# Kernel optimization log

Hardware: AMD Instinct MI355X
Metric: run time of the kernel (lower is better)

The kernel has to match this reference:

```python
import jax, jax.numpy as jnp
import numpy as np

B = 8192; N = 50; NUM_NODES = 200000; NUM_EDGES = 1000000
FEAT = 64; EFEAT = 4; TD = 16; D = 64


def setup_inputs() -> dict:
    key = jax.random.key(0)
    ks = jax.random.split(key, 32)
    p = lambda i, shape: jax.random.normal(ks[i], shape, jnp.float32) * 0.05
    inp = {}
    nf = jax.random.normal(ks[0], (NUM_NODES, FEAT), jnp.float32)
    skills = jax.random.randint(ks[1], (NUM_NODES,), 0, 100).astype(jnp.float32)
    inp['node_raw_features'] = nf.at[:, 0].set(skills)  # col 0 = skill id
    inp['edge_raw_features'] = jax.random.normal(ks[2], (NUM_EDGES, EFEAT), jnp.float32)
    inp['src_node_ids'] = jax.random.randint(ks[3], (B,), 0, NUM_NODES)
    inp['dst_node_ids'] = jax.random.randint(ks[4], (B,), 0, NUM_NODES)
    inp['node_interact_times'] = jax.random.uniform(ks[5], (B,), jnp.float32, 0.0, 1e4)
    inp['src_neighbor_node_ids'] = jax.random.randint(ks[6], (B, N), 0, NUM_NODES)
    inp['src_neighbor_edge_ids'] = jax.random.randint(ks[7], (B, N), 0, NUM_EDGES)
    inp['src_neighbor_times'] = jax.random.uniform(ks[8], (B, N), jnp.float32, 0.0, 1e4)
    inp['dst_neighbor_node_ids'] = jax.random.randint(ks[9], (B, N), 0, NUM_NODES)
    inp['dst_neighbor_edge_ids'] = jax.random.randint(ks[10], (B, N), 0, NUM_EDGES)
    inp['dst_neighbor_times'] = jax.random.uniform(ks[11], (B, N), jnp.float32, 0.0, 1e4)
    # projection layers
    inp['W_feat'] = p(12, (FEAT, D)); inp['b_feat'] = p(13, (D,))
    inp['W_edge'] = p(14, (1, D));    inp['b_edge'] = p(15, (D,))
    inp['W_time'] = p(16, (TD, D));   inp['b_time'] = p(17, (D,))
    inp['W_struct'] = p(18, (1, D));  inp['b_struct'] = p(19, (D,))
    inp['W_out'] = p(20, (D, D));     inp['b_out'] = p(21, (D,))
    # time encoder (cos(w*dt + b), trainable Linear(1, TD) as in TGN TimeEncoder)
    inp['time_w'] = p(22, (TD,)); inp['time_b'] = p(23, (TD,))
    # src / dst GRUs (PyTorch layout: W_ih [3H,E], W_hh [3H,H])
    inp['src_W_ih'] = p(24, (3 * D, D)); inp['src_W_hh'] = p(25, (3 * D, D))
    inp['src_b_ih'] = p(26, (3 * D,));   inp['src_b_hh'] = p(27, (3 * D,))
    inp['dst_W_ih'] = p(28, (3 * D, D)); inp['dst_W_hh'] = p(29, (3 * D, D))
    inp['dst_b_ih'] = p(30, (3 * D,));   inp['dst_b_hh'] = p(31, (3 * D,))
    return inp


def _lin(x, W, b):
    return x @ W + b


def _gru_last_hidden(x, W_ih, W_hh, b_ih, b_hh):
    # x: [B, T, E] -> final hidden state [B, H] (PyTorch GRU equations)
    Bb, _, _ = x.shape
    H = W_hh.shape[1]

    def step(h, xt):
        gi = xt @ W_ih.T + b_ih            # [B, 3H]
        gh = h @ W_hh.T + b_hh             # [B, 3H]
        ir, iz, inn = jnp.split(gi, 3, axis=-1)
        hr, hz, hn = jnp.split(gh, 3, axis=-1)
        r = jax.nn.sigmoid(ir + hr)
        z = jax.nn.sigmoid(iz + hz)
        n = jnp.tanh(inn + r * hn)
        h_new = (1.0 - z) * n + z * h
        return h_new, None

    h0 = jnp.zeros((Bb, H), x.dtype)
    hT, _ = jax.lax.scan(step, h0, jnp.swapaxes(x, 0, 1))
    return hT


def reference(node_raw_features, edge_raw_features, src_node_ids, dst_node_ids,
              node_interact_times, src_neighbor_node_ids, src_neighbor_edge_ids,
              src_neighbor_times, dst_neighbor_node_ids, dst_neighbor_edge_ids,
              dst_neighbor_times, W_feat, b_feat, W_edge, b_edge, W_time, b_time,
              W_struct, b_struct, W_out, b_out, time_w, time_b,
              src_W_ih, src_W_hh, src_b_ih, src_b_hh,
              dst_W_ih, dst_W_hh, dst_b_ih, dst_b_hh):
    t = node_interact_times
    # append the query interaction itself (edge id 0) -> [B, N+1]
    src_nids = jnp.concatenate([src_neighbor_node_ids, src_node_ids[:, None]], 1)
    src_eids = jnp.concatenate([src_neighbor_edge_ids, jnp.zeros_like(src_node_ids)[:, None]], 1)
    src_ts = jnp.concatenate([src_neighbor_times, t[:, None]], 1)
    dst_nids = jnp.concatenate([dst_neighbor_node_ids, dst_node_ids[:, None]], 1)
    dst_eids = jnp.concatenate([dst_neighbor_edge_ids, jnp.zeros_like(dst_node_ids)[:, None]], 1)
    dst_ts = jnp.concatenate([dst_neighbor_times, t[:, None]], 1)

    # co-occurrence features [B, N, 1]
    co_src = (src_neighbor_node_ids == dst_node_ids[:, None]).astype(jnp.float32)[..., None]
    co_dst = (dst_neighbor_node_ids == src_node_ids[:, None]).astype(jnp.float32)[..., None]
    # skill match features [B, N, 1]
    src_skill = node_raw_features[src_nids][:, :-1, 0].astype(jnp.int32)
    dst_skill = node_raw_features[dst_nids][:, -1, 0].astype(jnp.int32)[:, None]
    skill_f = (src_skill == dst_skill).astype(jnp.float32)[..., None]

    src_struct = _lin(co_src, W_struct, b_struct)
    dst_struct = _lin(co_dst, W_struct, b_struct)
    skill_struct = _lin(skill_f, W_struct, b_struct)

    def get_feats(nids, eids, ts):
        node_f = _lin(node_raw_features[nids], W_feat, b_feat)        # [B,N+1,D]
        delta = t[:, None] - ts                                       # dual-decay ablation: delta times
        tenc = jnp.cos(delta[..., None] * time_w + time_b)            # [B,N+1,TD]
        time_f = _lin(tenc, W_time, b_time)                           # [B,N+1,D]
        edge_f = _lin(edge_raw_features[eids][..., :1], W_edge, b_edge)
        return node_f, edge_f, time_f

    sn, se, st = get_feats(src_nids, src_eids, src_ts)
    dn, de, dt = get_feats(dst_nids, dst_eids, dst_ts)
    src_feats = sn + se + st
    dst_feats = dn + de + dt

    src_emb = _gru_last_hidden(src_feats[:, :-1] + skill_struct + src_struct,
                               src_W_ih, src_W_hh, src_b_ih, src_b_hh) + (se + st)[:, -1]
    dst_emb = _gru_last_hidden((de + dt)[:, :-1] + dst_struct,
                               dst_W_ih, dst_W_hh, dst_b_ih, dst_b_hh) + dst_feats[:, -1]

    return _lin(src_emb, W_out, b_out), _lin(dst_emb, W_out, b_out)
```

## Files before the change

### kernel.cpp

```cpp
#include <hip/hip_runtime.h>
#include <stdint.h>

#define BB 8192
#define NN 50

typedef _Float16 half8 __attribute__((ext_vector_type(8)));
typedef float floatx4 __attribute__((ext_vector_type(4)));

union FragU { uint4 u; half8 h; };
static __device__ __forceinline__ half8 u2h(uint4 u) { FragU f; f.u = u; return f.h; }

static __device__ __forceinline__ uint32_t pk2u(float a, float b) {
    auto p = __builtin_amdgcn_cvt_pkrtz(a, b);
    uint32_t u; __builtin_memcpy(&u, &p, 4); return u;
}

#define MFMA(A, B, C) __builtin_amdgcn_mfma_f32_16x16x32_f16((A), (B), (C), 0, 0, 0)

static __device__ __forceinline__ float fsig(float x)   { return 1.0f / (1.0f + __expf(-x)); }
static __device__ __forceinline__ float ftanhf(float x) { return 1.0f - 2.0f / (__expf(2.0f * x) + 1.0f); }

__global__ __launch_bounds__(256, 1)
void dygkt3(const float* __restrict__ nodef, const float* __restrict__ edgef,
            const int* __restrict__ src_ids, const int* __restrict__ dst_ids,
            const float* __restrict__ times,
            const int* __restrict__ s_nids, const int* __restrict__ s_eids,
            const float* __restrict__ s_ts,
            const int* __restrict__ d_nids, const int* __restrict__ d_eids,
            const float* __restrict__ d_ts,
            const float* __restrict__ W_feat, const float* __restrict__ b_feat,
            const float* __restrict__ W_edge, const float* __restrict__ b_edge,
            const float* __restrict__ W_time, const float* __restrict__ b_time,
            const float* __restrict__ W_str,  const float* __restrict__ b_str,
            const float* __restrict__ W_out,  const float* __restrict__ b_out,
            const float* __restrict__ time_w, const float* __restrict__ time_b,
            const float* __restrict__ sWih, const float* __restrict__ sWhh,
            const float* __restrict__ sbih, const float* __restrict__ sbhh,
            const float* __restrict__ dWih, const float* __restrict__ dWhh,
            const float* __restrict__ dbih, const float* __restrict__ dbhh,
            float* __restrict__ out)
{
    __shared__ uint4 wfA[8][64];
    __shared__ uint4 woA[8][64];
    __shared__ __align__(16) _Float16 xbuf[4][16 * 72];
    __shared__ __align__(16) _Float16 hbuf[4][16 * 72];

    const int tid = threadIdx.x, wave = tid >> 6, lane = tid & 63;
    const int g = lane >> 4, i16 = lane & 15;
    const bool is_src = blockIdx.x < 128;
    const int ib0 = (int)(blockIdx.x & 127) * 64 + wave * 16;
    const int b = ib0 + i16;

    for (int q = tid; q < 512; q += 256) {
        int l = q & 63, tt = q >> 6;
        int kh = tt >> 2, mt = tt & 3, gg = l >> 4, ii = l & 15;
        float v[8], w[8];
        #pragma unroll
        for (int j = 0; j < 8; ++j) {
            int k = 32 * kh + 8 * gg + j, m = 16 * mt + ii;
            v[j] = W_feat[k * 64 + m];
            w[j] = W_out[k * 64 + m];
        }
        wfA[tt][l] = make_uint4(pk2u(v[0],v[1]), pk2u(v[2],v[3]), pk2u(v[4],v[5]), pk2u(v[6],v[7]));
        woA[tt][l] = make_uint4(pk2u(w[0],w[1]), pk2u(w[2],w[3]), pk2u(w[4],w[5]), pk2u(w[6],w[7]));
    }
    for (int q = tid; q < 4 * 16 * 72 / 2; q += 256) ((uint32_t*)hbuf)[q] = 0;
    __syncthreads();

    const float* WI = is_src ? sWih : dWih;
    const float* WH = is_src ? sWhh : dWhh;
    uint4 wih[12][2], whh[12][2];
    #pragma unroll
    for (int mt = 0; mt < 12; ++mt)
        #pragma unroll
        for (int kh = 0; kh < 2; ++kh) {
            const float* p = WI + (size_t)(16 * mt + i16) * 64 + 32 * kh + 8 * g;
            float4 a = *(const float4*)p, c = *(const float4*)(p + 4);
            wih[mt][kh] = make_uint4(pk2u(a.x,a.y), pk2u(a.z,a.w), pk2u(c.x,c.y), pk2u(c.z,c.w));
            const float* q = WH + (size_t)(16 * mt + i16) * 64 + 32 * kh + 8 * g;
            float4 e = *(const float4*)q, f = *(const float4*)(q + 4);
            whh[mt][kh] = make_uint4(pk2u(e.x,e.y), pk2u(e.z,e.w), pk2u(f.x,f.y), pk2u(f.z,f.w));
        }

    uint4 wtA[4];
    #pragma unroll
    for (int mt = 0; mt < 4; ++mt) {
        float v[8];
        #pragma unroll
        for (int j = 0; j < 8; ++j) {
            int k = 8 * g + j, dim = 16 * mt + i16;
            float x = 0.0f;
            if (k < 16)       x = W_time[k * 64 + dim];
            else if (k == 16) x = W_edge[dim];
            else if (k == 17) x = W_str[dim];
            else if (k == 18) x = b_edge[dim] + b_time[dim];
            else if (k == 19) x = is_src ? (b_feat[dim] + 2.0f * b_str[dim]) : b_str[dim];
            else if (k == 20) x = b_feat[dim];
            v[j] = x;
        }
        wtA[mt] = make_uint4(pk2u(v[0],v[1]), pk2u(v[2],v[3]), pk2u(v[4],v[5]), pk2u(v[6],v[7]));
    }

    const float* BI = is_src ? sbih : dbih;
    const float* BH = is_src ? sbhh : dbhh;
    floatx4 brz[8], bin[4], bhn[4];
    #pragma unroll
    for (int mt = 0; mt < 8; ++mt) {
        floatx4 v;
        #pragma unroll
        for (int r = 0; r < 4; ++r) v[r] = BI[16 * mt + 4 * g + r] + BH[16 * mt + 4 * g + r];
        brz[mt] = v;
    }
    #pragma unroll
    for (int mt = 0; mt < 4; ++mt) {
        floatx4 vi, vh;
        #pragma unroll
        for (int r = 0; r < 4; ++r) {
            vi[r] = BI[128 + 16 * mt + 4 * g + r];
            vh[r] = BH[128 + 16 * mt + 4 * g + r];
        }
        bin[mt] = vi; bhn[mt] = vh;
    }

    const int* pn = (is_src ? s_nids : d_nids) + (size_t)b * NN;
    const int* pe = (is_src ? s_eids : d_eids) + (size_t)b * NN;
    const float* pt = (is_src ? s_ts : d_ts) + (size_t)b * NN;
    const float tqL = times[b];
    const int didL = dst_ids[b];
    const int oid = is_src ? didL : src_ids[b];
    const float dskill = is_src ? nodef[(size_t)didL * 64] : 0.0f;
    float twc[8], tbc[8];
    #pragma unroll
    for (int j = 0; j < 8; ++j) {
        int k = 8 * (g & 1) + j;
        twc[j] = time_w[k]; tbc[j] = time_b[k];
    }

    int nidC = pn[0], eidC = pe[0];
    float tsC = pt[0];
    float e0C = edgef[4 * (size_t)eidC];
    float4 nfa = {0,0,0,0}, nfb = {0,0,0,0}, nfc = {0,0,0,0}, nfd = {0,0,0,0};
    if (is_src) {
        const float* rp = nodef + (size_t)nidC * 64 + 8 * g;
        nfa = *(const float4*)rp;        nfb = *(const float4*)(rp + 4);
        nfc = *(const float4*)(rp + 32); nfd = *(const float4*)(rp + 36);
    }

    floatx4 hM[4] = {{0,0,0,0},{0,0,0,0},{0,0,0,0},{0,0,0,0}};
    const floatx4 z4 = {0,0,0,0};
    _Float16* xb = xbuf[wave];
    _Float16* hb = hbuf[wave];

    for (int t = 0; t < NN; ++t) {
        int nidN = 0, eidN = 0; float tsN = 0.0f;
        if (t + 1 < NN) { nidN = pn[t + 1]; eidN = pe[t + 1]; tsN = pt[t + 1]; }

        float nsk = __shfl(nfa.x, i16);
        float sf = ((nidC == oid) ? 1.0f : 0.0f) +
                   ((is_src && nsk == dskill) ? 1.0f : 0.0f);
        float delta = tqL - tsC;
        uint4 tb4;
        if (g < 2) {
            float cv[8];
            #pragma unroll
            for (int j = 0; j < 8; ++j) cv[j] = __cosf(delta * twc[j] + tbc[j]);
            tb4 = make_uint4(pk2u(cv[0],cv[1]), pk2u(cv[2],cv[3]), pk2u(cv[4],cv[5]), pk2u(cv[6],cv[7]));
        } else if (g == 2) {
            tb4 = make_uint4(pk2u(e0C, sf), pk2u(1.0f, 1.0f), 0u, 0u);
        } else {
            tb4 = make_uint4(0u, 0u, 0u, 0u);
        }
        half8 tB = u2h(tb4);

        floatx4 xacc[4];
        if (is_src) {
            uint4 nf0 = make_uint4(pk2u(nfa.x,nfa.y), pk2u(nfa.z,nfa.w), pk2u(nfb.x,nfb.y), pk2u(nfb.z,nfb.w));
            uint4 nf1 = make_uint4(pk2u(nfc.x,nfc.y), pk2u(nfc.z,nfc.w), pk2u(nfd.x,nfd.y), pk2u(nfd.z,nfd.w));
            half8 nB0 = u2h(nf0), nB1 = u2h(nf1);
            #pragma unroll
            for (int mt = 0; mt < 4; ++mt) {
                floatx4 a = MFMA(u2h(wfA[mt][lane]), nB0, z4);
                a = MFMA(u2h(wfA[4 + mt][lane]), nB1, a);
                xacc[mt] = MFMA(u2h(wtA[mt]), tB, a);
            }
        } else {
            #pragma unroll
            for (int mt = 0; mt < 4; ++mt) xacc[mt] = MFMA(u2h(wtA[mt]), tB, z4);
        }

        #pragma unroll
        for (int mt = 0; mt < 4; ++mt)
            *(uint2*)&xb[i16 * 72 + mt * 16 + 4 * g] =
                make_uint2(pk2u(xacc[mt][0], xacc[mt][1]), pk2u(xacc[mt][2], xacc[mt][3]));
        half8 xB0 = u2h(*(const uint4*)&xb[i16 * 72 + 8 * g]);
        half8 xB1 = u2h(*(const uint4*)&xb[i16 * 72 + 32 + 8 * g]);

        float e0N = 0.0f; float4 na = {0,0,0,0}, nb = {0,0,0,0}, nc = {0,0,0,0}, nd = {0,0,0,0};
        if (t + 1 < NN) {
            e0N = edgef[4 * (size_t)eidN];
            if (is_src) {
                const float* rp = nodef + (size_t)nidN * 64 + 8 * g;
                na = *(const float4*)rp;        nb = *(const float4*)(rp + 4);
                nc = *(const float4*)(rp + 32); nd = *(const float4*)(rp + 36);
            }
        }

        half8 hB0 = u2h(*(const uint4*)&hb[i16 * 72 + 8 * g]);
        half8 hB1 = u2h(*(const uint4*)&hb[i16 * 72 + 32 + 8 * g]);

        floatx4 rg[4], zg[4], ia[4], ha[4];
        #pragma unroll
        for (int mt = 0; mt < 4; ++mt) {
            floatx4 a = MFMA(u2h(wih[mt][0]), xB0, brz[mt]);
            a = MFMA(u2h(wih[mt][1]), xB1, a);
            a = MFMA(u2h(whh[mt][0]), hB0, a);
            rg[mt] = MFMA(u2h(whh[mt][1]), hB1, a);
        }
        #pragma unroll
        for (int mt = 0; mt < 4; ++mt) {
            floatx4 a = MFMA(u2h(wih[4 + mt][0]), xB0, brz[4 + mt]);
            a = MFMA(u2h(wih[4 + mt][1]), xB1, a);
            a = MFMA(u2h(whh[4 + mt][0]), hB0, a);
            zg[mt] = MFMA(u2h(whh[4 + mt][1]), hB1, a);
        }
        #pragma unroll
        for (int mt = 0; mt < 4; ++mt) {
            floatx4 a = MFMA(u2h(wih[8 + mt][0]), xB0, bin[mt]);
            ia[mt] = MFMA(u2h(wih[8 + mt][1]), xB1, a);
            floatx4 c = MFMA(u2h(whh[8 + mt][0]), hB0, bhn[mt]);
            ha[mt] = MFMA(u2h(whh[8 + mt][1]), hB1, c);
        }

        #pragma unroll
        for (int mt = 0; mt < 4; ++mt)
            #pragma unroll
            for (int r = 0; r < 4; ++r) {
                float rr = fsig(rg[mt][r]);
                float zz = fsig(zg[mt][r]);
                float nn = ftanhf(ia[mt][r] + rr * ha[mt][r]);
                hM[mt][r] = nn + zz * (hM[mt][r] - nn);
            }

        #pragma unroll
        for (int mt = 0; mt < 4; ++mt)
            *(uint2*)&hb[i16 * 72 + mt * 16 + 4 * g] =
                make_uint2(pk2u(hM[mt][0], hM[mt][1]), pk2u(hM[mt][2], hM[mt][3]));

        nidC = nidN; eidC = eidN; tsC = tsN; e0C = e0N;
        nfa = na; nfb = nb; nfc = nc; nfd = nd;
    }

    float e00 = edgef[0];
    uint4 tt4;
    if (g < 2) {
        float cv[8];
        #pragma unroll
        for (int j = 0; j < 8; ++j) cv[j] = __cosf(tbc[j]);
        tt4 = make_uint4(pk2u(cv[0],cv[1]), pk2u(cv[2],cv[3]), pk2u(cv[4],cv[5]), pk2u(cv[6],cv[7]));
    } else if (g == 2) {
        tt4 = make_uint4(pk2u(e00, 0.0f), pk2u(1.0f, 0.0f), pk2u(is_src ? 0.0f : 1.0f, 0.0f), 0u);
    } else {
        tt4 = make_uint4(0u, 0u, 0u, 0u);
    }
    half8 tT = u2h(tt4);

    floatx4 tacc[4];
    #pragma unroll
    for (int mt = 0; mt < 4; ++mt) tacc[mt] = MFMA(u2h(wtA[mt]), tT, z4);
    if (!is_src) {
        const float* rp = nodef + (size_t)didL * 64 + 8 * g;
        float4 da = *(const float4*)rp,        db = *(const float4*)(rp + 4);
        float4 dc = *(const float4*)(rp + 32), dd = *(const float4*)(rp + 36);
        uint4 d0 = make_uint4(pk2u(da.x,da.y), pk2u(da.z,da.w), pk2u(db.x,db.y), pk2u(db.z,db.w));
        uint4 d1 = make_uint4(pk2u(dc.x,dc.y), pk2u(dc.z,dc.w), pk2u(dd.x,dd.y), pk2u(dd.z,dd.w));
        #pragma unroll
        for (int mt = 0; mt < 4; ++mt) {
            tacc[mt] = MFMA(u2h(wfA[mt][lane]), u2h(d0), tacc[mt]);
            tacc[mt] = MFMA(u2h(wfA[4 + mt][lane]), u2h(d1), tacc[mt]);
        }
    }

    #pragma unroll
    for (int mt = 0; mt < 4; ++mt) {
        floatx4 e = hM[mt] + tacc[mt];
        *(uint2*)&xb[i16 * 72 + mt * 16 + 4 * g] =
            make_uint2(pk2u(e[0], e[1]), pk2u(e[2], e[3]));
    }
    half8 eB0 = u2h(*(const uint4*)&xb[i16 * 72 + 8 * g]);
    half8 eB1 = u2h(*(const uint4*)&xb[i16 * 72 + 32 + 8 * g]);

    const size_t obase = (is_src ? 0 : (size_t)BB * 64) + (size_t)(ib0 + i16) * 64;
    #pragma unroll
    for (int mt = 0; mt < 4; ++mt) {
        floatx4 bo;
        #pragma unroll
        for (int r = 0; r < 4; ++r) bo[r] = b_out[16 * mt + 4 * g + r];
        floatx4 o = MFMA(u2h(woA[mt][lane]), eB0, bo);
        o = MFMA(u2h(woA[4 + mt][lane]), eB1, o);
        #pragma unroll
        for (int r = 0; r < 4; ++r)
            out[obase + 16 * mt + 4 * g + r] = o[r];
    }
}

extern "C" void kernel_launch(void* const* d_in, const int* in_sizes, int n_in,
                              void* d_out, int out_size, void* d_ws, size_t ws_size,
                              hipStream_t stream) {
    (void)in_sizes; (void)n_in; (void)d_ws; (void)ws_size; (void)out_size;
    const float* nodef  = (const float*)d_in[0];
    const float* edgef  = (const float*)d_in[1];
    const int*   srcid  = (const int*)  d_in[2];
    const int*   dstid  = (const int*)  d_in[3];
    const float* times  = (const float*)d_in[4];
    const int*   s_nids = (const int*)  d_in[5];
    const int*   s_eids = (const int*)  d_in[6];
    const float* s_ts   = (const float*)d_in[7];
    const int*   d_nids = (const int*)  d_in[8];
    const int*   d_eids = (const int*)  d_in[9];
    const float* d_ts   = (const float*)d_in[10];
    const float* W_feat = (const float*)d_in[11];
    const float* b_feat = (const float*)d_in[12];
    const float* W_edge = (const float*)d_in[13];
    const float* b_edge = (const float*)d_in[14];
    const float* W_time = (const float*)d_in[15];
    const float* b_time = (const float*)d_in[16];
    const float* W_str  = (const float*)d_in[17];
    const float* b_str  = (const float*)d_in[18];
    const float* W_out  = (const float*)d_in[19];
    const float* b_out  = (const float*)d_in[20];
    const float* time_w = (const float*)d_in[21];
    const float* time_b = (const float*)d_in[22];
    const float* sWih   = (const float*)d_in[23];
    const float* sWhh   = (const float*)d_in[24];
    const float* sbih   = (const float*)d_in[25];
    const float* sbhh   = (const float*)d_in[26];
    const float* dWih   = (const float*)d_in[27];
    const float* dWhh   = (const float*)d_in[28];
    const float* dbih   = (const float*)d_in[29];
    const float* dbhh   = (const float*)d_in[30];

    dim3 grid(256), block(256);
    dygkt3<<<grid, block, 0, stream>>>(
        nodef, edgef, srcid, dstid, times,
        s_nids, s_eids, s_ts, d_nids, d_eids, d_ts,
        W_feat, b_feat, W_edge, b_edge, W_time, b_time,
        W_str, b_str, W_out, b_out, time_w, time_b,
        sWih, sWhh, sbih, sbhh, dWih, dWhh, dbih, dbhh,
        (float*)d_out);
}
```

Baseline: 300.4 us.

## Split each 16-row GRU batch across two waves with ping-pong LDS hidden state

Each 16-sample batch tile is now handled by a pair of waves. Each wave computes half of the 64 hidden units for every gate, and the halves are exchanged through double-buffered LDS with one barrier per timestep. This halves the per-wave MFMA chain on the serial recurrence and the register-resident weights, so more waves can run in parallel (1024 blocks of 128 threads, 2 blocks per CU). The cost is a block barrier every step. The change also switches sigmoid/tanh to exp2/rcp intrinsics and vectorizes the output store.

Measured after the change: 245.5 us. -18.3%, faster.

```diff
diff --git a/kernel.cpp b/kernel.cpp
--- a/kernel.cpp
+++ b/kernel.cpp
@@ -17,11 +17,30 @@
 
 #define MFMA(A, B, C) __builtin_amdgcn_mfma_f32_16x16x32_f16((A), (B), (C), 0, 0, 0)
 
-static __device__ __forceinline__ float fsig(float x)   { return 1.0f / (1.0f + __expf(-x)); }
-static __device__ __forceinline__ float ftanhf(float x) { return 1.0f - 2.0f / (__expf(2.0f * x) + 1.0f); }
-
-__global__ __launch_bounds__(256, 1)
-void dygkt3(const float* __restrict__ nodef, const float* __restrict__ edgef,
+static __device__ __forceinline__ float frcp(float x) {
+#if __has_builtin(__builtin_amdgcn_rcpf)
+    return __builtin_amdgcn_rcpf(x);
+#else
+    return 1.0f / x;
+#endif
+}
+static __device__ __forceinline__ float fexp2(float x) {
+#if __has_builtin(__builtin_amdgcn_exp2f)
+    return __builtin_amdgcn_exp2f(x);
+#else
+    return __expf(0.69314718056f * x);
+#endif
+}
+static __device__ __forceinline__ float fsig(float x)   { return frcp(1.0f + fexp2(-1.44269504089f * x)); }
+static __device__ __forceinline__ float ftanhf(float x) { return 1.0f - 2.0f * frcp(fexp2(2.88539008178f * x) + 1.0f); }
+
+static __device__ __forceinline__ void bar_lds() {
+    asm volatile("s_waitcnt lgkmcnt(0)" ::: "memory");
+    __builtin_amdgcn_s_barrier();
+}
+
+__global__ __launch_bounds__(128, 2)
+void dygkt4(const float* __restrict__ nodef, const float* __restrict__ edgef,
             const int* __restrict__ src_ids, const int* __restrict__ dst_ids,
             const float* __restrict__ times,
             const int* __restrict__ s_nids, const int* __restrict__ s_eids,
@@ -42,49 +61,53 @@
 {
     __shared__ uint4 wfA[8][64];
     __shared__ uint4 woA[8][64];
-    __shared__ __align__(16) _Float16 xbuf[4][16 * 72];
-    __shared__ __align__(16) _Float16 hbuf[4][16 * 72];
-
-    const int tid = threadIdx.x, wave = tid >> 6, lane = tid & 63;
+    __shared__ __align__(16) _Float16 xls[2][16 * 72];
+    __shared__ __align__(16) _Float16 hls[2][16 * 72];
+
+    const int tid = threadIdx.x, w = tid >> 6, lane = tid & 63;
     const int g = lane >> 4, i16 = lane & 15;
-    const bool is_src = blockIdx.x < 128;
-    const int ib0 = (int)(blockIdx.x & 127) * 64 + wave * 16;
+    const bool is_src = blockIdx.x < 512;
+    const int ib0 = (int)(blockIdx.x & 511) * 16;
     const int b = ib0 + i16;
 
-    for (int q = tid; q < 512; q += 256) {
+    for (int q = tid; q < 512; q += 128) {
         int l = q & 63, tt = q >> 6;
         int kh = tt >> 2, mt = tt & 3, gg = l >> 4, ii = l & 15;
-        float v[8], w[8];
+        float v[8], u[8];
         #pragma unroll
         for (int j = 0; j < 8; ++j) {
             int k = 32 * kh + 8 * gg + j, m = 16 * mt + ii;
             v[j] = W_feat[k * 64 + m];
-            w[j] = W_out[k * 64 + m];
+            u[j] = W_out[k * 64 + m];
         }
         wfA[tt][l] = make_uint4(pk2u(v[0],v[1]), pk2u(v[2],v[3]), pk2u(v[4],v[5]), pk2u(v[6],v[7]));
-        woA[tt][l] = make_uint4(pk2u(w[0],w[1]), pk2u(w[2],w[3]), pk2u(w[4],w[5]), pk2u(w[6],w[7]));
-    }
-    for (int q = tid; q < 4 * 16 * 72 / 2; q += 256) ((uint32_t*)hbuf)[q] = 0;
+        woA[tt][l] = make_uint4(pk2u(u[0],u[1]), pk2u(u[2],u[3]), pk2u(u[4],u[5]), pk2u(u[6],u[7]));
+    }
+    for (int q = tid; q < 16 * 72 / 2; q += 128) ((uint32_t*)hls[0])[q] = 0u;
     __syncthreads();
 
     const float* WI = is_src ? sWih : dWih;
     const float* WH = is_src ? sWhh : dWhh;
-    uint4 wih[12][2], whh[12][2];
-    #pragma unroll
-    for (int mt = 0; mt < 12; ++mt)
-        #pragma unroll
-        for (int kh = 0; kh < 2; ++kh) {
-            const float* p = WI + (size_t)(16 * mt + i16) * 64 + 32 * kh + 8 * g;
-            float4 a = *(const float4*)p, c = *(const float4*)(p + 4);
-            wih[mt][kh] = make_uint4(pk2u(a.x,a.y), pk2u(a.z,a.w), pk2u(c.x,c.y), pk2u(c.z,c.w));
-            const float* q = WH + (size_t)(16 * mt + i16) * 64 + 32 * kh + 8 * g;
-            float4 e = *(const float4*)q, f = *(const float4*)(q + 4);
-            whh[mt][kh] = make_uint4(pk2u(e.x,e.y), pk2u(e.z,e.w), pk2u(f.x,f.y), pk2u(f.z,f.w));
-        }
-
-    uint4 wtA[4];
-    #pragma unroll
-    for (int mt = 0; mt < 4; ++mt) {
+    uint4 wih[6][2], whh[6][2];
+    #pragma unroll
+    for (int gt = 0; gt < 3; ++gt)
+        #pragma unroll
+        for (int tq = 0; tq < 2; ++tq)
+            #pragma unroll
+            for (int kh = 0; kh < 2; ++kh) {
+                int row = 64 * gt + 16 * (2 * w + tq) + i16;
+                const float* p = WI + (size_t)row * 64 + 32 * kh + 8 * g;
+                float4 a = *(const float4*)p, c = *(const float4*)(p + 4);
+                wih[gt * 2 + tq][kh] = make_uint4(pk2u(a.x,a.y), pk2u(a.z,a.w), pk2u(c.x,c.y), pk2u(c.z,c.w));
+                const float* qq = WH + (size_t)row * 64 + 32 * kh + 8 * g;
+                float4 e = *(const float4*)qq, f = *(const float4*)(qq + 4);
+                whh[gt * 2 + tq][kh] = make_uint4(pk2u(e.x,e.y), pk2u(e.z,e.w), pk2u(f.x,f.y), pk2u(f.z,f.w));
+            }
+
+    uint4 wtA[2];
+    #pragma unroll
+    for (int tq = 0; tq < 2; ++tq) {
+        int mt = 2 * w + tq;
         float v[8];
         #pragma unroll
         for (int j = 0; j < 8; ++j) {
@@ -98,28 +121,29 @@
             else if (k == 20) x = b_feat[dim];
             v[j] = x;
         }
-        wtA[mt] = make_uint4(pk2u(v[0],v[1]), pk2u(v[2],v[3]), pk2u(v[4],v[5]), pk2u(v[6],v[7]));
+        wtA[tq] = make_uint4(pk2u(v[0],v[1]), pk2u(v[2],v[3]), pk2u(v[4],v[5]), pk2u(v[6],v[7]));
     }
 
     const float* BI = is_src ? sbih : dbih;
     const float* BH = is_src ? sbhh : dbhh;
-    floatx4 brz[8], bin[4], bhn[4];
-    #pragma unroll
-    for (int mt = 0; mt < 8; ++mt) {
-        floatx4 v;
-        #pragma unroll
-        for (int r = 0; r < 4; ++r) v[r] = BI[16 * mt + 4 * g + r] + BH[16 * mt + 4 * g + r];
-        brz[mt] = v;
-    }
-    #pragma unroll
-    for (int mt = 0; mt < 4; ++mt) {
+    floatx4 brz[4], bin[2], bhn[2];
+    #pragma unroll
+    for (int gz = 0; gz < 2; ++gz)
+        #pragma unroll
+        for (int tq = 0; tq < 2; ++tq) {
+            int r0 = 64 * gz + 16 * (2 * w + tq) + 4 * g;
+            floatx4 v;
+            #pragma unroll
+            for (int r = 0; r < 4; ++r) v[r] = BI[r0 + r] + BH[r0 + r];
+            brz[gz * 2 + tq] = v;
+        }
+    #pragma unroll
+    for (int tq = 0; tq < 2; ++tq) {
+        int r0 = 128 + 16 * (2 * w + tq) + 4 * g;
         floatx4 vi, vh;
         #pragma unroll
-        for (int r = 0; r < 4; ++r) {
-            vi[r] = BI[128 + 16 * mt + 4 * g + r];
-            vh[r] = BH[128 + 16 * mt + 4 * g + r];
-        }
-        bin[mt] = vi; bhn[mt] = vh;
+        for (int r = 0; r < 4; ++r) { vi[r] = BI[r0 + r]; vh[r] = BH[r0 + r]; }
+        bin[tq] = vi; bhn[tq] = vh;
     }
 
     const int* pn = (is_src ? s_nids : d_nids) + (size_t)b * NN;
@@ -146,10 +170,9 @@
         nfc = *(const float4*)(rp + 32); nfd = *(const float4*)(rp + 36);
     }
 
-    floatx4 hM[4] = {{0,0,0,0},{0,0,0,0},{0,0,0,0},{0,0,0,0}};
+    floatx4 hM[2] = {{0,0,0,0},{0,0,0,0}};
     const floatx4 z4 = {0,0,0,0};
-    _Float16* xb = xbuf[wave];
-    _Float16* hb = hbuf[wave];
+    int cur = 0;
 
     for (int t = 0; t < NN; ++t) {
         int nidN = 0, eidN = 0; float tsN = 0.0f;
@@ -172,28 +195,27 @@
         }
         half8 tB = u2h(tb4);
 
-        floatx4 xacc[4];
+        floatx4 xacc[2];
         if (is_src) {
             uint4 nf0 = make_uint4(pk2u(nfa.x,nfa.y), pk2u(nfa.z,nfa.w), pk2u(nfb.x,nfb.y), pk2u(nfb.z,nfb.w));
             uint4 nf1 = make_uint4(pk2u(nfc.x,nfc.y), pk2u(nfc.z,nfc.w), pk2u(nfd.x,nfd.y), pk2u(nfd.z,nfd.w));
             half8 nB0 = u2h(nf0), nB1 = u2h(nf1);
             #pragma unroll
-            for (int mt = 0; mt < 4; ++mt) {
+            for (int tq = 0; tq < 2; ++tq) {
+                int mt = 2 * w + tq;
                 floatx4 a = MFMA(u2h(wfA[mt][lane]), nB0, z4);
                 a = MFMA(u2h(wfA[4 + mt][lane]), nB1, a);
-                xacc[mt] = MFMA(u2h(wtA[mt]), tB, a);
+                xacc[tq] = MFMA(u2h(wtA[tq]), tB, a);
             }
         } else {
             #pragma unroll
-            for (int mt = 0; mt < 4; ++mt) xacc[mt] = MFMA(u2h(wtA[mt]), tB, z4);
-        }
-
-        #pragma unroll
-        for (int mt = 0; mt < 4; ++mt)
-            *(uint2*)&xb[i16 * 72 + mt * 16 + 4 * g] =
-                make_uint2(pk2u(xacc[mt][0], xacc[mt][1]), pk2u(xacc[mt][2], xacc[mt][3]));
-        half8 xB0 = u2h(*(const uint4*)&xb[i16 * 72 + 8 * g]);
-        half8 xB1 = u2h(*(const uint4*)&xb[i16 * 72 + 32 + 8 * g]);
+            for (int tq = 0; tq < 2; ++tq) xacc[tq] = MFMA(u2h(wtA[tq]), tB, z4);
+        }
+
+        #pragma unroll
+        for (int tq = 0; tq < 2; ++tq)
+            *(uint2*)&xls[cur][i16 * 72 + 32 * w + 16 * tq + 4 * g] =
+                make_uint2(pk2u(xacc[tq][0], xacc[tq][1]), pk2u(xacc[tq][2], xacc[tq][3]));
 
         float e0N = 0.0f; float4 na = {0,0,0,0}, nb = {0,0,0,0}, nc = {0,0,0,0}, nd = {0,0,0,0};
         if (t + 1 < NN) {
@@ -205,47 +227,52 @@
             }
         }
 
-        half8 hB0 = u2h(*(const uint4*)&hb[i16 * 72 + 8 * g]);
-        half8 hB1 = u2h(*(const uint4*)&hb[i16 * 72 + 32 + 8 * g]);
-
-        floatx4 rg[4], zg[4], ia[4], ha[4];
-        #pragma unroll
-        for (int mt = 0; mt < 4; ++mt) {
-            floatx4 a = MFMA(u2h(wih[mt][0]), xB0, brz[mt]);
-            a = MFMA(u2h(wih[mt][1]), xB1, a);
-            a = MFMA(u2h(whh[mt][0]), hB0, a);
-            rg[mt] = MFMA(u2h(whh[mt][1]), hB1, a);
-        }
-        #pragma unroll
-        for (int mt = 0; mt < 4; ++mt) {
-            floatx4 a = MFMA(u2h(wih[4 + mt][0]), xB0, brz[4 + mt]);
-            a = MFMA(u2h(wih[4 + mt][1]), xB1, a);
-            a = MFMA(u2h(whh[4 + mt][0]), hB0, a);
-            zg[mt] = MFMA(u2h(whh[4 + mt][1]), hB1, a);
-        }
-        #pragma unroll
-        for (int mt = 0; mt < 4; ++mt) {
-            floatx4 a = MFMA(u2h(wih[8 + mt][0]), xB0, bin[mt]);
-            ia[mt] = MFMA(u2h(wih[8 + mt][1]), xB1, a);
-            floatx4 c = MFMA(u2h(whh[8 + mt][0]), hB0, bhn[mt]);
-            ha[mt] = MFMA(u2h(whh[8 + mt][1]), hB1, c);
-        }
-
-        #pragma unroll
-        for (int mt = 0; mt < 4; ++mt)
+        bar_lds();
+
+        half8 xB0 = u2h(*(const uint4*)&xls[cur][i16 * 72 + 8 * g]);
+        half8 xB1 = u2h(*(const uint4*)&xls[cur][i16 * 72 + 32 + 8 * g]);
+        half8 hB0 = u2h(*(const uint4*)&hls[cur][i16 * 72 + 8 * g]);
+        half8 hB1 = u2h(*(const uint4*)&hls[cur][i16 * 72 + 32 + 8 * g]);
+
+        floatx4 rg[2], zg[2], ia[2], ha[2];
+        #pragma unroll
+        for (int tq = 0; tq < 2; ++tq) {
+            floatx4 a = MFMA(u2h(wih[tq][0]), xB0, brz[tq]);
+            a = MFMA(u2h(wih[tq][1]), xB1, a);
+            a = MFMA(u2h(whh[tq][0]), hB0, a);
+            rg[tq] = MFMA(u2h(whh[tq][1]), hB1, a);
+        }
+        #pragma unroll
+        for (int tq = 0; tq < 2; ++tq) {
+            floatx4 a = MFMA(u2h(wih[2 + tq][0]), xB0, brz[2 + tq]);
+            a = MFMA(u2h(wih[2 + tq][1]), xB1, a);
+            a = MFMA(u2h(whh[2 + tq][0]), hB0, a);
+            zg[tq] = MFMA(u2h(whh[2 + tq][1]), hB1, a);
+        }
+        #pragma unroll
+        for (int tq = 0; tq < 2; ++tq) {
+            floatx4 a = MFMA(u2h(wih[4 + tq][0]), xB0, bin[tq]);
+            ia[tq] = MFMA(u2h(wih[4 + tq][1]), xB1, a);
+            floatx4 c = MFMA(u2h(whh[4 + tq][0]), hB0, bhn[tq]);
+            ha[tq] = MFMA(u2h(whh[4 + tq][1]), hB1, c);
+        }
+
+        #pragma unroll
+        for (int tq = 0; tq < 2; ++tq)
             #pragma unroll
             for (int r = 0; r < 4; ++r) {
-                float rr = fsig(rg[mt][r]);
-                float zz = fsig(zg[mt][r]);
-                float nn = ftanhf(ia[mt][r] + rr * ha[mt][r]);
-                hM[mt][r] = nn + zz * (hM[mt][r] - nn);
+                float rr = fsig(rg[tq][r]);
+                float zz = fsig(zg[tq][r]);
+                float nn = ftanhf(ia[tq][r] + rr * ha[tq][r]);
+                hM[tq][r] = nn + zz * (hM[tq][r] - nn);
             }
 
         #pragma unroll
-        for (int mt = 0; mt < 4; ++mt)
-            *(uint2*)&hb[i16 * 72 + mt * 16 + 4 * g] =
-                make_uint2(pk2u(hM[mt][0], hM[mt][1]), pk2u(hM[mt][2], hM[mt][3]));
-
+        for (int tq = 0; tq < 2; ++tq)
+            *(uint2*)&hls[cur ^ 1][i16 * 72 + 32 * w + 16 * tq + 4 * g] =
+                make_uint2(pk2u(hM[tq][0], hM[tq][1]), pk2u(hM[tq][2], hM[tq][3]));
+
+        cur ^= 1;
         nidC = nidN; eidC = eidN; tsC = tsN; e0C = e0N;
         nfa = na; nfb = nb; nfc = nc; nfd = nd;
     }
@@ -264,9 +291,9 @@
     }
     half8 tT = u2h(tt4);
 
-    floatx4 tacc[4];
-    #pragma unroll
-    for (int mt = 0; mt < 4; ++mt) tacc[mt] = MFMA(u2h(wtA[mt]), tT, z4);
+    floatx4 tacc[2];
+    #pragma unroll
+    for (int tq = 0; tq < 2; ++tq) tacc[tq] = MFMA(u2h(wtA[tq]), tT, z4);
     if (!is_src) {
         const float* rp = nodef + (size_t)didL * 64 + 8 * g;
         float4 da = *(const float4*)rp,        db = *(const float4*)(rp + 4);
@@ -274,32 +301,33 @@
         uint4 d0 = make_uint4(pk2u(da.x,da.y), pk2u(da.z,da.w), pk2u(db.x,db.y), pk2u(db.z,db.w));
         uint4 d1 = make_uint4(pk2u(dc.x,dc.y), pk2u(dc.z,dc.w), pk2u(dd.x,dd.y), pk2u(dd.z,dd.w));
         #pragma unroll
-        for (int mt = 0; mt < 4; ++mt) {
-            tacc[mt] = MFMA(u2h(wfA[mt][lane]), u2h(d0), tacc[mt]);
-            tacc[mt] = MFMA(u2h(wfA[4 + mt][lane]), u2h(d1), tacc[mt]);
-        }
-    }
-
-    #pragma unroll
-    for (int mt = 0; mt < 4; ++mt) {
-        floatx4 e = hM[mt] + tacc[mt];
-        *(uint2*)&xb[i16 * 72 + mt * 16 + 4 * g] =
+        for (int tq = 0; tq < 2; ++tq) {
+            int mt = 2 * w + tq;
+            tacc[tq] = MFMA(u2h(wfA[mt][lane]), u2h(d0), tacc[tq]);
+            tacc[tq] = MFMA(u2h(wfA[4 + mt][lane]), u2h(d1), tacc[tq]);
+        }
+    }
+
+    #pragma unroll
+    for (int tq = 0; tq < 2; ++tq) {
+        floatx4 e = hM[tq] + tacc[tq];
+        *(uint2*)&xls[0][i16 * 72 + 32 * w + 16 * tq + 4 * g] =
             make_uint2(pk2u(e[0], e[1]), pk2u(e[2], e[3]));
     }
-    half8 eB0 = u2h(*(const uint4*)&xb[i16 * 72 + 8 * g]);
-    half8 eB1 = u2h(*(const uint4*)&xb[i16 * 72 + 32 + 8 * g]);
-
-    const size_t obase = (is_src ? 0 : (size_t)BB * 64) + (size_t)(ib0 + i16) * 64;
-    #pragma unroll
-    for (int mt = 0; mt < 4; ++mt) {
+    bar_lds();
+    half8 eB0 = u2h(*(const uint4*)&xls[0][i16 * 72 + 8 * g]);
+    half8 eB1 = u2h(*(const uint4*)&xls[0][i16 * 72 + 32 + 8 * g]);
+
+    const size_t obase = (is_src ? 0 : (size_t)BB * 64) + (size_t)b * 64;
+    #pragma unroll
+    for (int tq = 0; tq < 2; ++tq) {
+        int mt = 2 * w + tq;
         floatx4 bo;
         #pragma unroll
         for (int r = 0; r < 4; ++r) bo[r] = b_out[16 * mt + 4 * g + r];
         floatx4 o = MFMA(u2h(woA[mt][lane]), eB0, bo);
         o = MFMA(u2h(woA[4 + mt][lane]), eB1, o);
-        #pragma unroll
-        for (int r = 0; r < 4; ++r)
-            out[obase + 16 * mt + 4 * g + r] = o[r];
+        *(floatx4*)(out + obase + 16 * mt + 4 * g) = o;
     }
 }
 
@@ -339,8 +367,8 @@
     const float* dbih   = (const float*)d_in[29];
     const float* dbhh   = (const float*)d_in[30];
 
-    dim3 grid(256), block(256);
-    dygkt3<<<grid, block, 0, stream>>>(
+    dim3 grid(1024), block(128);
+    dygkt4<<<grid, block, 0, stream>>>(
         nodef, edgef, srcid, dstid, times,
         s_nids, s_eids, s_ts, d_nids, d_eids, d_ts,
         W_feat, b_feat, W_edge, b_edge, W_time, b_time,
```

## Halve per-wave batch to 8 rows, move W_ih to LDS, fold gate scales into weights

Applied to the files above, without the earlier changes.

Each wave now handles 8 batch rows instead of 16, so the grid doubles to 512 blocks and launch bounds allow 2 blocks per CU. This trades wasted MFMA columns for more parallelism on the sequential GRU recurrence. W_ih, the time/edge weights and the biases move from registers to shared memory to free VGPRs. The sigmoid and tanh scale factors (log2e) are folded into the weights and biases so gates use raw exp2 and rcp builtins. Other changes: the output projection reads W_out from global memory directly, and the dst node row is prefetched in the last loop iteration.

After: 737.6 us. 146% more time.

```diff
diff --git a/kernel.cpp b/kernel.cpp
--- a/kernel.cpp
+++ b/kernel.cpp
@@ -17,11 +17,23 @@
 
 #define MFMA(A, B, C) __builtin_amdgcn_mfma_f32_16x16x32_f16((A), (B), (C), 0, 0, 0)
 
-static __device__ __forceinline__ float fsig(float x)   { return 1.0f / (1.0f + __expf(-x)); }
-static __device__ __forceinline__ float ftanhf(float x) { return 1.0f - 2.0f / (__expf(2.0f * x) + 1.0f); }
-
-__global__ __launch_bounds__(256, 1)
-void dygkt3(const float* __restrict__ nodef, const float* __restrict__ edgef,
+static __device__ __forceinline__ float frcp(float x) {
+#if __has_builtin(__builtin_amdgcn_rcpf)
+    return __builtin_amdgcn_rcpf(x);
+#else
+    return 1.0f / x;
+#endif
+}
+static __device__ __forceinline__ float fexp2(float x) {
+#if __has_builtin(__builtin_amdgcn_exp2f)
+    return __builtin_amdgcn_exp2f(x);
+#else
+    return __expf(0.69314718056f * x);
+#endif
+}
+
+__global__ __launch_bounds__(256, 2)
+void dygkt9(const float* __restrict__ nodef, const float* __restrict__ edgef,
             const int* __restrict__ src_ids, const int* __restrict__ dst_ids,
             const float* __restrict__ times,
             const int* __restrict__ s_nids, const int* __restrict__ s_eids,
@@ -40,55 +52,44 @@
             const float* __restrict__ dbih, const float* __restrict__ dbhh,
             float* __restrict__ out)
 {
+    __shared__ uint4 wihL[24][64];
     __shared__ uint4 wfA[8][64];
-    __shared__ uint4 woA[8][64];
-    __shared__ __align__(16) _Float16 xbuf[4][16 * 72];
-    __shared__ __align__(16) _Float16 hbuf[4][16 * 72];
-
-    const int tid = threadIdx.x, wave = tid >> 6, lane = tid & 63;
-    const int g = lane >> 4, i16 = lane & 15;
-    const bool is_src = blockIdx.x < 128;
-    const int ib0 = (int)(blockIdx.x & 127) * 64 + wave * 16;
-    const int b = ib0 + i16;
+    __shared__ uint4 wtAL[4][64];
+    __shared__ floatx4 biasL[16][4];
+    __shared__ __align__(16) _Float16 xtr[4][9 * 72];
+    __shared__ __align__(16) _Float16 htr[4][9 * 72];
+
+    const int tid = threadIdx.x, w = tid >> 6, lane = tid & 63;
+    const int g = lane >> 4, i16 = lane & 15, i8 = lane & 7;
+    const int ri = (i16 < 8) ? i16 : 8;
+    const bool is_src = (blockIdx.x & 1) == 0;
+    const int b = (int)(blockIdx.x >> 1) * 32 + w * 8 + i8;
+
+    const float SRZ = -1.44269504089f;
+    const float SN  =  2.88539008178f;
+    const floatx4 z4 = {0, 0, 0, 0};
+
+    const float* WI = is_src ? sWih : dWih;
+    const float* WH = is_src ? sWhh : dWhh;
+    const float* BI = is_src ? sbih : dbih;
+    const float* BH = is_src ? sbhh : dbhh;
 
     for (int q = tid; q < 512; q += 256) {
         int l = q & 63, tt = q >> 6;
         int kh = tt >> 2, mt = tt & 3, gg = l >> 4, ii = l & 15;
-        float v[8], w[8];
+        float v[8];
+        #pragma unroll
+        for (int j = 0; j < 8; ++j)
+            v[j] = W_feat[(32 * kh + 8 * gg + j) * 64 + 16 * mt + ii];
+        wfA[tt][l] = make_uint4(pk2u(v[0],v[1]), pk2u(v[2],v[3]), pk2u(v[4],v[5]), pk2u(v[6],v[7]));
+    }
+    {
+        int l = tid & 63, mt = tid >> 6;
+        int gg = l >> 4, ii = l & 15;
+        float v[8];
         #pragma unroll
         for (int j = 0; j < 8; ++j) {
-            int k = 32 * kh + 8 * gg + j, m = 16 * mt + ii;
-            v[j] = W_feat[k * 64 + m];
-            w[j] = W_out[k * 64 + m];
-        }
-        wfA[tt][l] = make_uint4(pk2u(v[0],v[1]), pk2u(v[2],v[3]), pk2u(v[4],v[5]), pk2u(v[6],v[7]));
-        woA[tt][l] = make_uint4(pk2u(w[0],w[1]), pk2u(w[2],w[3]), pk2u(w[4],w[5]), pk2u(w[6],w[7]));
-    }
-    for (int q = tid; q < 4 * 16 * 72 / 2; q += 256) ((uint32_t*)hbuf)[q] = 0;
-    __syncthreads();
-
-    const float* WI = is_src ? sWih : dWih;
-    const float* WH = is_src ? sWhh : dWhh;
-    uint4 wih[12][2], whh[12][2];
-    #pragma unroll
-    for (int mt = 0; mt < 12; ++mt)
-        #pragma unroll
-        for (int kh = 0; kh < 2; ++kh) {
-            const float* p = WI + (size_t)(16 * mt + i16) * 64 + 32 * kh + 8 * g;
-            float4 a = *(const float4*)p, c = *(const float4*)(p + 4);
-            wih[mt][kh] = make_uint4(pk2u(a.x,a.y), pk2u(a.z,a.w), pk2u(c.x,c.y), pk2u(c.z,c.w));
-            const float* q = WH + (size_t)(16 * mt + i16) * 64 + 32 * kh + 8 * g;
-            float4 e = *(const float4*)q, f = *(const float4*)(q + 4);
-            whh[mt][kh] = make_uint4(pk2u(e.x,e.y), pk2u(e.z,e.w), pk2u(f.x,f.y), pk2u(f.z,f.w));
-        }
-
-    uint4 wtA[4];
-    #pragma unroll
-    for (int mt = 0; mt < 4; ++mt) {
-        float v[8];
-        #pragma unroll
-        for (int j = 0; j < 8; ++j) {
-            int k = 8 * g + j, dim = 16 * mt + i16;
+            int k = 8 * gg + j, dim = 16 * mt + ii;
             float x = 0.0f;
             if (k < 16)       x = W_time[k * 64 + dim];
             else if (k == 16) x = W_edge[dim];
@@ -98,28 +99,51 @@
             else if (k == 20) x = b_feat[dim];
             v[j] = x;
         }
-        wtA[mt] = make_uint4(pk2u(v[0],v[1]), pk2u(v[2],v[3]), pk2u(v[4],v[5]), pk2u(v[6],v[7]));
-    }
-
-    const float* BI = is_src ? sbih : dbih;
-    const float* BH = is_src ? sbhh : dbhh;
-    floatx4 brz[8], bin[4], bhn[4];
-    #pragma unroll
-    for (int mt = 0; mt < 8; ++mt) {
+        wtAL[mt][l] = make_uint4(pk2u(v[0],v[1]), pk2u(v[2],v[3]), pk2u(v[4],v[5]), pk2u(v[6],v[7]));
+    }
+    for (int q = tid; q < 1536; q += 256) {
+        int l = q & 63, idx = q >> 6;
+        int gt = idx >> 3, rem = idx & 7, mt = rem >> 1, kh = rem & 1;
+        float s = (gt == 2) ? SN : SRZ;
+        int gg = l >> 4, ii = l & 15;
+        int row = 64 * gt + 16 * mt + ii;
+        const float* p = WI + (size_t)row * 64 + 32 * kh + 8 * gg;
+        float4 a = *(const float4*)p, c = *(const float4*)(p + 4);
+        wihL[idx][l] = make_uint4(pk2u(s*a.x,s*a.y), pk2u(s*a.z,s*a.w),
+                                  pk2u(s*c.x,s*c.y), pk2u(s*c.z,s*c.w));
+    }
+    if (tid < 64) {
+        int idx = tid >> 2, gg = tid & 3;
+        int which = idx >> 2, mt = idx & 3;
+        int base = 16 * mt + 4 * gg;
         floatx4 v;
         #pragma unroll
-        for (int r = 0; r < 4; ++r) v[r] = BI[16 * mt + 4 * g + r] + BH[16 * mt + 4 * g + r];
-        brz[mt] = v;
-    }
-    #pragma unroll
-    for (int mt = 0; mt < 4; ++mt) {
-        floatx4 vi, vh;
-        #pragma unroll
         for (int r = 0; r < 4; ++r) {
-            vi[r] = BI[128 + 16 * mt + 4 * g + r];
-            vh[r] = BH[128 + 16 * mt + 4 * g + r];
-        }
-        bin[mt] = vi; bhn[mt] = vh;
+            float x;
+            if (which == 0)      x = SRZ * (BI[base + r] + BH[base + r]);
+            else if (which == 1) x = SRZ * (BI[64 + base + r] + BH[64 + base + r]);
+            else if (which == 2) x = SN * BI[128 + base + r];
+            else                 x = SN * BH[128 + base + r];
+            v[r] = x;
+        }
+        biasL[idx][gg] = v;
+    }
+    for (int q = tid; q < 4 * 9 * 72 / 2; q += 256) ((uint32_t*)htr)[q] = 0u;
+
+    uint4 whh[3][4][2];
+    #pragma unroll
+    for (int gt = 0; gt < 3; ++gt) {
+        const float s = (gt == 2) ? SN : SRZ;
+        #pragma unroll
+        for (int mt = 0; mt < 4; ++mt)
+            #pragma unroll
+            for (int kh = 0; kh < 2; ++kh) {
+                int row = 64 * gt + 16 * mt + i16;
+                const float* p = WH + (size_t)row * 64 + 32 * kh + 8 * g;
+                float4 a = *(const float4*)p, c = *(const float4*)(p + 4);
+                whh[gt][mt][kh] = make_uint4(pk2u(s*a.x,s*a.y), pk2u(s*a.z,s*a.w),
+                                             pk2u(s*c.x,s*c.y), pk2u(s*c.z,s*c.w));
+            }
     }
 
     const int* pn = (is_src ? s_nids : d_nids) + (size_t)b * NN;
@@ -136,6 +160,8 @@
         twc[j] = time_w[k]; tbc[j] = time_b[k];
     }
 
+    __syncthreads();
+
     int nidC = pn[0], eidC = pe[0];
     float tsC = pt[0];
     float e0C = edgef[4 * (size_t)eidC];
@@ -146,16 +172,15 @@
         nfc = *(const float4*)(rp + 32); nfd = *(const float4*)(rp + 36);
     }
 
-    floatx4 hM[4] = {{0,0,0,0},{0,0,0,0},{0,0,0,0},{0,0,0,0}};
-    const floatx4 z4 = {0,0,0,0};
-    _Float16* xb = xbuf[wave];
-    _Float16* hb = hbuf[wave];
+    floatx4 hM[4] = {z4, z4, z4, z4};
+    _Float16* xp = xtr[w];
+    _Float16* hp = htr[w];
 
     for (int t = 0; t < NN; ++t) {
         int nidN = 0, eidN = 0; float tsN = 0.0f;
         if (t + 1 < NN) { nidN = pn[t + 1]; eidN = pe[t + 1]; tsN = pt[t + 1]; }
 
-        float nsk = __shfl(nfa.x, i16);
+        float nsk = __shfl(nfa.x, i8);
         float sf = ((nidC == oid) ? 1.0f : 0.0f) +
                    ((is_src && nsk == dskill) ? 1.0f : 0.0f);
         float delta = tqL - tsC;
@@ -172,7 +197,6 @@
         }
         half8 tB = u2h(tb4);
 
-        floatx4 xacc[4];
         if (is_src) {
             uint4 nf0 = make_uint4(pk2u(nfa.x,nfa.y), pk2u(nfa.z,nfa.w), pk2u(nfb.x,nfb.y), pk2u(nfb.z,nfb.w));
             uint4 nf1 = make_uint4(pk2u(nfc.x,nfc.y), pk2u(nfc.z,nfc.w), pk2u(nfd.x,nfd.y), pk2u(nfd.z,nfd.w));
@@ -181,19 +205,18 @@
             for (int mt = 0; mt < 4; ++mt) {
                 floatx4 a = MFMA(u2h(wfA[mt][lane]), nB0, z4);
                 a = MFMA(u2h(wfA[4 + mt][lane]), nB1, a);
-                xacc[mt] = MFMA(u2h(wtA[mt]), tB, a);
+                a = MFMA(u2h(wtAL[mt][lane]), tB, a);
+                *(uint2*)&xp[ri * 72 + 16 * mt + 4 * g] =
+                    make_uint2(pk2u(a[0], a[1]), pk2u(a[2], a[3]));
             }
         } else {
             #pragma unroll
-            for (int mt = 0; mt < 4; ++mt) xacc[mt] = MFMA(u2h(wtA[mt]), tB, z4);
-        }
-
-        #pragma unroll
-        for (int mt = 0; mt < 4; ++mt)
-            *(uint2*)&xb[i16 * 72 + mt * 16 + 4 * g] =
-                make_uint2(pk2u(xacc[mt][0], xacc[mt][1]), pk2u(xacc[mt][2], xacc[mt][3]));
-        half8 xB0 = u2h(*(const uint4*)&xb[i16 * 72 + 8 * g]);
-        half8 xB1 = u2h(*(const uint4*)&xb[i16 * 72 + 32 + 8 * g]);
+            for (int mt = 0; mt < 4; ++mt) {
+                floatx4 a = MFMA(u2h(wtAL[mt][lane]), tB, z4);
+                *(uint2*)&xp[ri * 72 + 16 * mt + 4 * g] =
+                    make_uint2(pk2u(a[0], a[1]), pk2u(a[2], a[3]));
+            }
+        }
 
         float e0N = 0.0f; float4 na = {0,0,0,0}, nb = {0,0,0,0}, nc = {0,0,0,0}, nd = {0,0,0,0};
         if (t + 1 < NN) {
@@ -203,48 +226,41 @@
                 na = *(const float4*)rp;        nb = *(const float4*)(rp + 4);
                 nc = *(const float4*)(rp + 32); nd = *(const float4*)(rp + 36);
             }
-        }
-
-        half8 hB0 = u2h(*(const uint4*)&hb[i16 * 72 + 8 * g]);
-        half8 hB1 = u2h(*(const uint4*)&hb[i16 * 72 + 32 + 8 * g]);
-
-        floatx4 rg[4], zg[4], ia[4], ha[4];
+        } else if (!is_src) {
+            const float* rp = nodef + (size_t)didL * 64 + 8 * g;
+            na = *(const float4*)rp;        nb = *(const float4*)(rp + 4);
+            nc = *(const float4*)(rp + 32); nd = *(const float4*)(rp + 36);
+        }
+
+        half8 xB0 = u2h(*(const uint4*)&xp[i8 * 72 + 8 * g]);
+        half8 xB1 = u2h(*(const uint4*)&xp[i8 * 72 + 32 + 8 * g]);
+        half8 hB0 = u2h(*(const uint4*)&hp[i8 * 72 + 8 * g]);
+        half8 hB1 = u2h(*(const uint4*)&hp[i8 * 72 + 32 + 8 * g]);
+
         #pragma unroll
         for (int mt = 0; mt < 4; ++mt) {
-            floatx4 a = MFMA(u2h(wih[mt][0]), xB0, brz[mt]);
-            a = MFMA(u2h(wih[mt][1]), xB1, a);
-            a = MFMA(u2h(whh[mt][0]), hB0, a);
-            rg[mt] = MFMA(u2h(whh[mt][1]), hB1, a);
-        }
-        #pragma unroll
-        for (int mt = 0; mt < 4; ++mt) {
-            floatx4 a = MFMA(u2h(wih[4 + mt][0]), xB0, brz[4 + mt]);
-            a = MFMA(u2h(wih[4 + mt][1]), xB1, a);
-            a = MFMA(u2h(whh[4 + mt][0]), hB0, a);
-            zg[mt] = MFMA(u2h(whh[4 + mt][1]), hB1, a);
-        }
-        #pragma unroll
-        for (int mt = 0; mt < 4; ++mt) {
-            floatx4 a = MFMA(u2h(wih[8 + mt][0]), xB0, bin[mt]);
-            ia[mt] = MFMA(u2h(wih[8 + mt][1]), xB1, a);
-            floatx4 c = MFMA(u2h(whh[8 + mt][0]), hB0, bhn[mt]);
-            ha[mt] = MFMA(u2h(whh[8 + mt][1]), hB1, c);
-        }
-
-        #pragma unroll
-        for (int mt = 0; mt < 4; ++mt)
+            floatx4 rg = MFMA(u2h(wihL[2 * mt + 0][lane]), xB0, biasL[mt][g]);
+            rg = MFMA(u2h(wihL[2 * mt + 1][lane]), xB1, rg);
+            rg = MFMA(u2h(whh[0][mt][0]), hB0, rg);
+            rg = MFMA(u2h(whh[0][mt][1]), hB1, rg);
+            floatx4 zg = MFMA(u2h(wihL[8 + 2 * mt + 0][lane]), xB0, biasL[4 + mt][g]);
+            zg = MFMA(u2h(wihL[8 + 2 * mt + 1][lane]), xB1, zg);
+            zg = MFMA(u2h(whh[1][mt][0]), hB0, zg);
+            zg = MFMA(u2h(whh[1][mt][1]), hB1, zg);
+            floatx4 ia = MFMA(u2h(wihL[16 + 2 * mt + 0][lane]), xB0, biasL[8 + mt][g]);
+            ia = MFMA(u2h(wihL[16 + 2 * mt + 1][lane]), xB1, ia);
+            floatx4 ha = MFMA(u2h(whh[2][mt][0]), hB0, biasL[12 + mt][g]);
+            ha = MFMA(u2h(whh[2][mt][1]), hB1, ha);
             #pragma unroll
             for (int r = 0; r < 4; ++r) {
-                float rr = fsig(rg[mt][r]);
-                float zz = fsig(zg[mt][r]);
-                float nn = ftanhf(ia[mt][r] + rr * ha[mt][r]);
+                float rr = frcp(1.0f + fexp2(rg[r]));
+                float zz = frcp(1.0f + fexp2(zg[r]));
+                float nn = 1.0f - 2.0f * frcp(fexp2(ia[r] + rr * ha[r]) + 1.0f);
                 hM[mt][r] = nn + zz * (hM[mt][r] - nn);
             }
-
-        #pragma unroll
-        for (int mt = 0; mt < 4; ++mt)
-            *(uint2*)&hb[i16 * 72 + mt * 16 + 4 * g] =
+            *(uint2*)&hp[ri * 72 + 16 * mt + 4 * g] =
                 make_uint2(pk2u(hM[mt][0], hM[mt][1]), pk2u(hM[mt][2], hM[mt][3]));
+        }
 
         nidC = nidN; eidC = eidN; tsC = tsN; e0C = e0N;
         nfa = na; nfb = nb; nfc = nc; nfd = nd;
@@ -266,13 +282,10 @@
 
     floatx4 tacc[4];
     #pragma unroll
-    for (int mt = 0; mt < 4; ++mt) tacc[mt] = MFMA(u2h(wtA[mt]), tT, z4);
+    for (int mt = 0; mt < 4; ++mt) tacc[mt] = MFMA(u2h(wtAL[mt][lane]), tT, z4);
     if (!is_src) {
-        const float* rp = nodef + (size_t)didL * 64 + 8 * g;
-        float4 da = *(const float4*)rp,        db = *(const float4*)(rp + 4);
-        float4 dc = *(const float4*)(rp + 32), dd = *(const float4*)(rp + 36);
-        uint4 d0 = make_uint4(pk2u(da.x,da.y), pk2u(da.z,da.w), pk2u(db.x,db.y), pk2u(db.z,db.w));
-        uint4 d1 = make_uint4(pk2u(dc.x,dc.y), pk2u(dc.z,dc.w), pk2u(dd.x,dd.y), pk2u(dd.z,dd.w));
+        uint4 d0 = make_uint4(pk2u(nfa.x,nfa.y), pk2u(nfa.z,nfa.w), pk2u(nfb.x,nfb.y), pk2u(nfb.z,nfb.w));
+        uint4 d1 = make_uint4(pk2u(nfc.x,nfc.y), pk2u(nfc.z,nfc.w), pk2u(nfd.x,nfd.y), pk2u(nfd.z,nfd.w));
         #pragma unroll
         for (int mt = 0; mt < 4; ++mt) {
             tacc[mt] = MFMA(u2h(wfA[mt][lane]), u2h(d0), tacc[mt]);
@@ -283,23 +296,31 @@
     #pragma unroll
     for (int mt = 0; mt < 4; ++mt) {
         floatx4 e = hM[mt] + tacc[mt];
-        *(uint2*)&xb[i16 * 72 + mt * 16 + 4 * g] =
+        *(uint2*)&xp[ri * 72 + 16 * mt + 4 * g] =
             make_uint2(pk2u(e[0], e[1]), pk2u(e[2], e[3]));
     }
-    half8 eB0 = u2h(*(const uint4*)&xb[i16 * 72 + 8 * g]);
-    half8 eB1 = u2h(*(const uint4*)&xb[i16 * 72 + 32 + 8 * g]);
-
-    const size_t obase = (is_src ? 0 : (size_t)BB * 64) + (size_t)(ib0 + i16) * 64;
+    half8 eB0 = u2h(*(const uint4*)&xp[i8 * 72 + 8 * g]);
+    half8 eB1 = u2h(*(const uint4*)&xp[i8 * 72 + 32 + 8 * g]);
+
+    const size_t obase = (is_src ? 0 : (size_t)BB * 64) + (size_t)b * 64;
     #pragma unroll
     for (int mt = 0; mt < 4; ++mt) {
+        float v[8], u[8];
+        #pragma unroll
+        for (int j = 0; j < 8; ++j) {
+            int m = 16 * mt + i16;
+            v[j] = W_out[(8 * g + j) * 64 + m];
+            u[j] = W_out[(32 + 8 * g + j) * 64 + m];
+        }
+        uint4 wo0 = make_uint4(pk2u(v[0],v[1]), pk2u(v[2],v[3]), pk2u(v[4],v[5]), pk2u(v[6],v[7]));
+        uint4 wo1 = make_uint4(pk2u(u[0],u[1]), pk2u(u[2],u[3]), pk2u(u[4],u[5]), pk2u(u[6],u[7]));
         floatx4 bo;
         #pragma unroll
         for (int r = 0; r < 4; ++r) bo[r] = b_out[16 * mt + 4 * g + r];
-        floatx4 o = MFMA(u2h(woA[mt][lane]), eB0, bo);
-        o = MFMA(u2h(woA[4 + mt][lane]), eB1, o);
-        #pragma unroll
-        for (int r = 0; r < 4; ++r)
-            out[obase + 16 * mt + 4 * g + r] = o[r];
+        floatx4 o = MFMA(u2h(wo0), eB0, bo);
+        o = MFMA(u2h(wo1), eB1, o);
+        if (i16 < 8)
+            *(floatx4*)(out + obase + 16 * mt + 4 * g) = o;
     }
 }
 
@@ -339,8 +360,8 @@
     const float* dbih   = (const float*)d_in[29];
     const float* dbhh   = (const float*)d_in[30];
 
-    dim3 grid(256), block(256);
-    dygkt3<<<grid, block, 0, stream>>>(
+    dim3 grid(512), block(256);
+    dygkt9<<<grid, block, 0, stream>>>(
         nodef, edgef, srcid, dstid, times,
         s_nids, s_eids, s_ts, d_nids, d_eids, d_ts,
         W_feat, b_feat, W_edge, b_edge, W_time, b_time,
```
